# Optimization experiments

Measured on AMD Instinct MI355X. Metric: run time of the kernel, lower is better.

The kernel has to match this reference:

```python
import jax, jax.numpy as jnp
import numpy as np

B, N, E, C_IN, C_OUT = 4, 50000, 800000, 128, 128


def setup_inputs() -> dict:
    key = jax.random.key(0)
    k1, k2, k3, k4, k5 = jax.random.split(key, 5)
    x = jax.random.normal(k1, (B, N, C_IN), dtype=jnp.float32)
    edge_row = jax.random.randint(k2, (E,), 0, N, dtype=jnp.int32)
    edge_col = jax.random.randint(k3, (E,), 0, N, dtype=jnp.int32)
    edge_vals = jax.random.uniform(k4, (E,), dtype=jnp.float32)
    W = jax.random.normal(k5, (C_IN, C_OUT), dtype=jnp.float32) * 0.1  # weight_stddev=0.1
    b = jnp.full((C_OUT,), 0.1, dtype=jnp.float32)  # bias_constant=0.1
    return {"x": x, "edge_row": edge_row, "edge_col": edge_col,
            "edge_vals": edge_vals, "W": W, "b": b}


def reference(x, edge_row, edge_col, edge_vals, W, b):
    # Sparse adjacency aggregation: agg[b, r, :] = sum_e vals[e] * x[b, col[e], :]
    n = x.shape[1]

    def spmm(xb):  # xb: [N, C_in]
        msgs = xb[edge_col] * edge_vals[:, None]          # [E, C_in]
        return jax.ops.segment_sum(msgs, edge_row, num_segments=n)  # [N, C_in]

    agg = jax.vmap(spmm)(x)                               # [B, N, C_in]
    out = jnp.einsum('bnc,co->bno', agg, W) + b           # dense GEMM + bias
    return jax.nn.relu(out)
```

## Files before the change

### kernel.cpp

```cpp
#include <hip/hip_runtime.h>

#define NROWS 50000
#define BATCH 4
#define CH    128
#define CAP   64

typedef float  f32x4  __attribute__((ext_vector_type(4)));
typedef __bf16 bf16x8 __attribute__((ext_vector_type(8)));
typedef short  s16x8  __attribute__((ext_vector_type(8)));

static __device__ __forceinline__ unsigned short f2bf(float f) {
    unsigned u = __builtin_bit_cast(unsigned, f);
    u += 0x7fffu + ((u >> 16) & 1u);
    return (unsigned short)(u >> 16);
}

__global__ void k_scatter(const int* __restrict__ row, const int* __restrict__ col,
                          const float* __restrict__ vals, int E,
                          int* __restrict__ cnt, unsigned long long* __restrict__ csr) {
    int e = blockIdx.x * blockDim.x + threadIdx.x;
    if (e < E) {
        int r = row[e];
        int p = atomicAdd(&cnt[r], 1);
        if (p < CAP) {
            unsigned long long pk =
                (unsigned long long)(unsigned)col[e] |
                ((unsigned long long)__builtin_bit_cast(unsigned, vals[e]) << 32);
            csr[r * CAP + p] = pk;
        }
    }
}

__global__ __launch_bounds__(256) void k_xw(const float* __restrict__ x,
                                            const float* __restrict__ W,
                                            unsigned short* __restrict__ y) {
    __shared__ unsigned short WtL[128 * 136];
    __shared__ unsigned short yt[4][16 * 136];
    const int tid = threadIdx.x;
    for (int idx = tid; idx < 128 * 128; idx += 256) {
        int k = idx >> 7, n = idx & 127;
        WtL[n * 136 + k] = f2bf(W[idx]);
    }
    __syncthreads();

    const int wave = tid >> 6;
    const int lane = tid & 63;
    const int m    = lane & 15;
    const int quad = lane >> 4;
    unsigned short* __restrict__ myt = yt[wave];

    const int NSTRIP = (BATCH * NROWS) / 64;
    for (int s = blockIdx.x; s < NSTRIP; s += gridDim.x) {
        const int row0 = s * 64 + wave * 16;

        s16x8 a_s[4];
        const float* xr = x + (size_t)(row0 + m) * CH;
        #pragma unroll
        for (int kk = 0; kk < 4; ++kk) {
            const float4* p = (const float4*)(xr + kk * 32 + quad * 8);
            float4 f0 = p[0], f1 = p[1];
            s16x8 sv;
            sv[0] = f2bf(f0.x); sv[1] = f2bf(f0.y); sv[2] = f2bf(f0.z); sv[3] = f2bf(f0.w);
            sv[4] = f2bf(f1.x); sv[5] = f2bf(f1.y); sv[6] = f2bf(f1.z); sv[7] = f2bf(f1.w);
            a_s[kk] = sv;
        }

        #pragma unroll
        for (int nt = 0; nt < 8; ++nt) {
            f32x4 acc = {0.f, 0.f, 0.f, 0.f};
            #pragma unroll
            for (int kk = 0; kk < 4; ++kk) {
                bf16x8 b = *(const bf16x8*)&WtL[(nt * 16 + m) * 136 + kk * 32 + quad * 8];
                acc = __builtin_amdgcn_mfma_f32_16x16x32_bf16(
                          __builtin_bit_cast(bf16x8, a_s[kk]), b, acc, 0, 0, 0);
            }
            #pragma unroll
            for (int reg = 0; reg < 4; ++reg)
                myt[(quad * 4 + reg) * 136 + nt * 16 + m] = f2bf(acc[reg]);
        }

        #pragma unroll
        for (int it = 0; it < 4; ++it) {
            const int lrow = it * 4 + (lane >> 4);
            const int seg  = lane & 15;
            uint4 v = *(const uint4*)&myt[lrow * 136 + seg * 8];
            const int i  = row0 + lrow;
            const int bb = i / NROWS;
            const int n  = i - bb * NROWS;
            *(uint4*)&y[((size_t)n * BATCH + bb) * CH + seg * 8] = v;
        }
    }
}

template<int B0>
__global__ __launch_bounds__(128) void k_spmm_h(const unsigned* __restrict__ y,
                                                const int* __restrict__ cnt,
                                                const unsigned long long* __restrict__ csr,
                                                const float* __restrict__ bias,
                                                float* __restrict__ out) {
    __shared__ unsigned long long lcsr[CAP];
    const int r    = blockIdx.x;
    const int tid  = threadIdx.x;
    const int b    = B0 + (tid >> 6);
    const int lane = tid & 63;
    const int deg  = min(cnt[r], CAP);
    if (tid < deg) lcsr[tid] = csr[r * CAP + tid];
    __syncthreads();

    const unsigned* __restrict__ Y = y + b * (CH / 2) + lane;
    float ax = 0.f, ay = 0.f;
    int e = 0;
    for (; e + 8 <= deg; e += 8) {
        unsigned long long pk[8];
        unsigned u[8];
        #pragma unroll
        for (int j = 0; j < 8; ++j) pk[j] = lcsr[e + j];
        #pragma unroll
        for (int j = 0; j < 8; ++j) u[j] = Y[(size_t)(unsigned)pk[j] * 256];
        #pragma unroll
        for (int j = 0; j < 8; ++j) {
            float v = __builtin_bit_cast(float, (unsigned)(pk[j] >> 32));
            ax += v * __builtin_bit_cast(float, u[j] << 16);
            ay += v * __builtin_bit_cast(float, u[j] & 0xffff0000u);
        }
    }
    for (; e < deg; ++e) {
        unsigned long long pk = lcsr[e];
        float v = __builtin_bit_cast(float, (unsigned)(pk >> 32));
        unsigned u = Y[(size_t)(unsigned)pk * 256];
        ax += v * __builtin_bit_cast(float, u << 16);
        ay += v * __builtin_bit_cast(float, u & 0xffff0000u);
    }

    float2 bv = ((const float2*)bias)[lane];
    float ox = fmaxf(ax + bv.x, 0.f);
    float oy = fmaxf(ay + bv.y, 0.f);
    unsigned long long packed =
        (unsigned long long)__builtin_bit_cast(unsigned, ox) |
        ((unsigned long long)__builtin_bit_cast(unsigned, oy) << 32);
    unsigned long long* dst =
        (unsigned long long*)(out + ((size_t)b * NROWS + r) * CH) + lane;
    __builtin_nontemporal_store(packed, dst);
}

extern "C" void kernel_launch(void* const* d_in, const int* in_sizes, int n_in,
                              void* d_out, int out_size, void* d_ws, size_t ws_size,
                              hipStream_t stream) {
    const float* x        = (const float*)d_in[0];
    const int*   edge_row = (const int*)d_in[1];
    const int*   edge_col = (const int*)d_in[2];
    const float* edge_val = (const float*)d_in[3];
    const float* W        = (const float*)d_in[4];
    const float* bias     = (const float*)d_in[5];
    float*       out      = (float*)d_out;

    const int E = in_sizes[1];

    int*                cnt = (int*)d_ws;
    unsigned long long* csr = (unsigned long long*)(cnt + 50048);
    unsigned short*     y   = (unsigned short*)(csr + (size_t)NROWS * CAP);

    hipMemsetAsync(cnt, 0, 50048 * sizeof(int), stream);
    k_scatter<<<(E + 255) / 256, 256, 0, stream>>>(edge_row, edge_col, edge_val, E,
                                                   cnt, csr);
    k_xw<<<1250, 256, 0, stream>>>(x, W, y);
    k_spmm_h<0><<<NROWS, 128, 0, stream>>>((const unsigned*)y, cnt, csr, bias, out);
    k_spmm_h<2><<<NROWS, 128, 0, stream>>>((const unsigned*)y, cnt, csr, bias, out);
}
```

Before: 362.8 us.

## Write permuted bf16 layout from MFMA registers and fuse batch SpMM kernels

The XW kernel drops its LDS transpose staging and writes MFMA accumulator results directly to global memory in a permuted bf16 pair layout. The SpMM is merged into one kernel in which each wave handles one row across all four batches, with each lane gathering a 16-byte uint4 per edge instead of 4 bytes. This replaces two launches that each read the CSR, and the wider gather should cut gather instruction count. In exchange, output stores become scattered 4-byte nontemporal writes instead of 8-byte coalesced ones, and the strided channel permutation adds more complex indexing.

```diff
diff --git a/kernel.cpp b/kernel.cpp
--- a/kernel.cpp
+++ b/kernel.cpp
@@ -13,6 +13,9 @@
     unsigned u = __builtin_bit_cast(unsigned, f);
     u += 0x7fffu + ((u >> 16) & 1u);
     return (unsigned short)(u >> 16);
+}
+static __device__ __forceinline__ unsigned packbf(float lo, float hi) {
+    return (unsigned)f2bf(lo) | ((unsigned)f2bf(hi) << 16);
 }
 
 __global__ void k_scatter(const int* __restrict__ row, const int* __restrict__ col,
@@ -31,11 +34,10 @@
     }
 }
 
-__global__ __launch_bounds__(256) void k_xw(const float* __restrict__ x,
-                                            const float* __restrict__ W,
-                                            unsigned short* __restrict__ y) {
+__global__ __launch_bounds__(256, 4) void k_xw(const float* __restrict__ x,
+                                               const float* __restrict__ W,
+                                               unsigned* __restrict__ y) {
     __shared__ unsigned short WtL[128 * 136];
-    __shared__ unsigned short yt[4][16 * 136];
     const int tid = threadIdx.x;
     for (int idx = tid; idx < 128 * 128; idx += 256) {
         int k = idx >> 7, n = idx & 127;
@@ -47,7 +49,6 @@
     const int lane = tid & 63;
     const int m    = lane & 15;
     const int quad = lane >> 4;
-    unsigned short* __restrict__ myt = yt[wave];
 
     const int NSTRIP = (BATCH * NROWS) / 64;
     for (int s = blockIdx.x; s < NSTRIP; s += gridDim.x) {
@@ -65,82 +66,104 @@
             a_s[kk] = sv;
         }
 
+        unsigned uc[4][4];
         #pragma unroll
-        for (int nt = 0; nt < 8; ++nt) {
-            f32x4 acc = {0.f, 0.f, 0.f, 0.f};
+        for (int np = 0; np < 4; ++np) {
+            f32x4 acc0 = {0.f, 0.f, 0.f, 0.f};
+            f32x4 acc1 = {0.f, 0.f, 0.f, 0.f};
             #pragma unroll
             for (int kk = 0; kk < 4; ++kk) {
-                bf16x8 b = *(const bf16x8*)&WtL[(nt * 16 + m) * 136 + kk * 32 + quad * 8];
-                acc = __builtin_amdgcn_mfma_f32_16x16x32_bf16(
-                          __builtin_bit_cast(bf16x8, a_s[kk]), b, acc, 0, 0, 0);
+                bf16x8 b0 = *(const bf16x8*)&WtL[((2 * np) * 16 + m) * 136 + kk * 32 + quad * 8];
+                acc0 = __builtin_amdgcn_mfma_f32_16x16x32_bf16(
+                           __builtin_bit_cast(bf16x8, a_s[kk]), b0, acc0, 0, 0, 0);
+            }
+            #pragma unroll
+            for (int kk = 0; kk < 4; ++kk) {
+                bf16x8 b1 = *(const bf16x8*)&WtL[((2 * np + 1) * 16 + m) * 136 + kk * 32 + quad * 8];
+                acc1 = __builtin_amdgcn_mfma_f32_16x16x32_bf16(
+                           __builtin_bit_cast(bf16x8, a_s[kk]), b1, acc1, 0, 0, 0);
             }
             #pragma unroll
             for (int reg = 0; reg < 4; ++reg)
-                myt[(quad * 4 + reg) * 136 + nt * 16 + m] = f2bf(acc[reg]);
+                uc[reg][np] = packbf(acc0[reg], acc1[reg]);
         }
 
         #pragma unroll
-        for (int it = 0; it < 4; ++it) {
-            const int lrow = it * 4 + (lane >> 4);
-            const int seg  = lane & 15;
-            uint4 v = *(const uint4*)&myt[lrow * 136 + seg * 8];
-            const int i  = row0 + lrow;
+        for (int reg = 0; reg < 4; ++reg) {
+            const int i  = row0 + quad * 4 + reg;
             const int bb = i / NROWS;
             const int n  = i - bb * NROWS;
-            *(uint4*)&y[((size_t)n * BATCH + bb) * CH + seg * 8] = v;
+            uint4 v;
+            v.x = uc[reg][0]; v.y = uc[reg][1]; v.z = uc[reg][2]; v.w = uc[reg][3];
+            *(uint4*)&y[((size_t)n * 4 + bb) * 64 + m * 4] = v;
         }
     }
 }
 
-template<int B0>
-__global__ __launch_bounds__(128) void k_spmm_h(const unsigned* __restrict__ y,
-                                                const int* __restrict__ cnt,
-                                                const unsigned long long* __restrict__ csr,
-                                                const float* __restrict__ bias,
-                                                float* __restrict__ out) {
-    __shared__ unsigned long long lcsr[CAP];
-    const int r    = blockIdx.x;
+__global__ __launch_bounds__(256) void k_spmm(const uint4* __restrict__ y4,
+                                              const int* __restrict__ cnt,
+                                              const unsigned long long* __restrict__ csr,
+                                              const float* __restrict__ bias,
+                                              float* __restrict__ out) {
+    __shared__ unsigned long long lcsr[4][CAP];
     const int tid  = threadIdx.x;
-    const int b    = B0 + (tid >> 6);
+    const int wave = tid >> 6;
     const int lane = tid & 63;
+    const int b    = lane >> 4;
+    const int m    = lane & 15;
+    const int r    = blockIdx.x * 4 + wave;
     const int deg  = min(cnt[r], CAP);
-    if (tid < deg) lcsr[tid] = csr[r * CAP + tid];
+    if (lane < deg) lcsr[wave][lane] = csr[(size_t)r * CAP + lane];
     __syncthreads();
 
-    const unsigned* __restrict__ Y = y + b * (CH / 2) + lane;
-    float ax = 0.f, ay = 0.f;
+    const uint4* __restrict__ Yl = y4 + lane;
+    float ax[4] = {0.f, 0.f, 0.f, 0.f};
+    float ay[4] = {0.f, 0.f, 0.f, 0.f};
+
     int e = 0;
     for (; e + 8 <= deg; e += 8) {
         unsigned long long pk[8];
-        unsigned u[8];
         #pragma unroll
-        for (int j = 0; j < 8; ++j) pk[j] = lcsr[e + j];
+        for (int j = 0; j < 8; ++j) pk[j] = lcsr[wave][e + j];
+        uint4 u[8];
         #pragma unroll
-        for (int j = 0; j < 8; ++j) u[j] = Y[(size_t)(unsigned)pk[j] * 256];
+        for (int j = 0; j < 8; ++j) u[j] = Yl[(size_t)(unsigned)pk[j] * 64];
         #pragma unroll
         for (int j = 0; j < 8; ++j) {
             float v = __builtin_bit_cast(float, (unsigned)(pk[j] >> 32));
-            ax += v * __builtin_bit_cast(float, u[j] << 16);
-            ay += v * __builtin_bit_cast(float, u[j] & 0xffff0000u);
+            ax[0] += v * __builtin_bit_cast(float, u[j].x << 16);
+            ay[0] += v * __builtin_bit_cast(float, u[j].x & 0xffff0000u);
+            ax[1] += v * __builtin_bit_cast(float, u[j].y << 16);
+            ay[1] += v * __builtin_bit_cast(float, u[j].y & 0xffff0000u);
+            ax[2] += v * __builtin_bit_cast(float, u[j].z << 16);
+            ay[2] += v * __builtin_bit_cast(float, u[j].z & 0xffff0000u);
+            ax[3] += v * __builtin_bit_cast(float, u[j].w << 16);
+            ay[3] += v * __builtin_bit_cast(float, u[j].w & 0xffff0000u);
         }
     }
     for (; e < deg; ++e) {
-        unsigned long long pk = lcsr[e];
+        unsigned long long pk = lcsr[wave][e];
         float v = __builtin_bit_cast(float, (unsigned)(pk >> 32));
-        unsigned u = Y[(size_t)(unsigned)pk * 256];
-        ax += v * __builtin_bit_cast(float, u << 16);
-        ay += v * __builtin_bit_cast(float, u & 0xffff0000u);
+        uint4 u = Yl[(size_t)(unsigned)pk * 64];
+        ax[0] += v * __builtin_bit_cast(float, u.x << 16);
+        ay[0] += v * __builtin_bit_cast(float, u.x & 0xffff0000u);
+        ax[1] += v * __builtin_bit_cast(float, u.y << 16);
+        ay[1] += v * __builtin_bit_cast(float, u.y & 0xffff0000u);
+        ax[2] += v * __builtin_bit_cast(float, u.z << 16);
+        ay[2] += v * __builtin_bit_cast(float, u.z & 0xffff0000u);
+        ax[3] += v * __builtin_bit_cast(float, u.w << 16);
+        ay[3] += v * __builtin_bit_cast(float, u.w & 0xffff0000u);
     }
 
-    float2 bv = ((const float2*)bias)[lane];
-    float ox = fmaxf(ax + bv.x, 0.f);
-    float oy = fmaxf(ay + bv.y, 0.f);
-    unsigned long long packed =
-        (unsigned long long)__builtin_bit_cast(unsigned, ox) |
-        ((unsigned long long)__builtin_bit_cast(unsigned, oy) << 32);
-    unsigned long long* dst =
-        (unsigned long long*)(out + ((size_t)b * NROWS + r) * CH) + lane;
-    __builtin_nontemporal_store(packed, dst);
+    float* __restrict__ orow = out + ((size_t)b * NROWS + r) * CH;
+    #pragma unroll
+    for (int j = 0; j < 4; ++j) {
+        const int c0 = m + 32 * j;
+        float ox = fmaxf(ax[j] + bias[c0], 0.f);
+        float oy = fmaxf(ay[j] + bias[c0 + 16], 0.f);
+        __builtin_nontemporal_store(ox, orow + c0);
+        __builtin_nontemporal_store(oy, orow + c0 + 16);
+    }
 }
 
 extern "C" void kernel_launch(void* const* d_in, const int* in_sizes, int n_in,
@@ -158,12 +181,11 @@
 
     int*                cnt = (int*)d_ws;
     unsigned long long* csr = (unsigned long long*)(cnt + 50048);
-    unsigned short*     y   = (unsigned short*)(csr + (size_t)NROWS * CAP);
+    unsigned*           y   = (unsigned*)(csr + (size_t)NROWS * CAP);
 
     hipMemsetAsync(cnt, 0, 50048 * sizeof(int), stream);
     k_scatter<<<(E + 255) / 256, 256, 0, stream>>>(edge_row, edge_col, edge_val, E,
                                                    cnt, csr);
     k_xw<<<1250, 256, 0, stream>>>(x, W, y);
-    k_spmm_h<0><<<NROWS, 128, 0, stream>>>((const unsigned*)y, cnt, csr, bias, out);
-    k_spmm_h<2><<<NROWS, 128, 0, stream>>>((const unsigned*)y, cnt, csr, bias, out);
+    k_spmm<<<NROWS / 4, 256, 0, stream>>>((const uint4*)y, cnt, csr, bias, out);
 }
```

Result: slower. 402.1 us (+10.8%).

## Merge batch-split SpMM kernels into one wave-per-row kernel with 16-byte gathers

Applied to the files above, without the earlier changes.

Replaces the two half-batch SpMM launches, which used one block per row and 4-byte gathers, with a single launch where each wave owns one row. Each wave covers all four batches using 16-byte uint4 gathers from the bf16 Y buffer, so one 1 KB row of Y is read in a single load per lane. The CSR list is loaded once instead of twice, and launch count drops. Results are staged through shared memory so the output stores stay coalesced. The trade-off is more registers per lane and the extra shared-memory staging step.

```diff
diff --git a/kernel.cpp b/kernel.cpp
--- a/kernel.cpp
+++ b/kernel.cpp
@@ -92,55 +92,78 @@
     }
 }
 
-template<int B0>
-__global__ __launch_bounds__(128) void k_spmm_h(const unsigned* __restrict__ y,
-                                                const int* __restrict__ cnt,
-                                                const unsigned long long* __restrict__ csr,
-                                                const float* __restrict__ bias,
-                                                float* __restrict__ out) {
-    __shared__ unsigned long long lcsr[CAP];
-    const int r    = blockIdx.x;
+__global__ __launch_bounds__(256) void k_spmm(const uint4* __restrict__ y4,
+                                              const int* __restrict__ cnt,
+                                              const unsigned long long* __restrict__ csr,
+                                              const float* __restrict__ bias,
+                                              float* __restrict__ out) {
+    __shared__ unsigned long long lcsr[4][CAP];
+    __shared__ float lout[4][512];
     const int tid  = threadIdx.x;
-    const int b    = B0 + (tid >> 6);
+    const int wave = tid >> 6;
     const int lane = tid & 63;
+    const int b    = lane >> 4;
+    const int m    = lane & 15;
+    const int r    = blockIdx.x * 4 + wave;
     const int deg  = min(cnt[r], CAP);
-    if (tid < deg) lcsr[tid] = csr[r * CAP + tid];
+    if (lane < deg) lcsr[wave][lane] = csr[(size_t)r * CAP + lane];
     __syncthreads();
 
-    const unsigned* __restrict__ Y = y + b * (CH / 2) + lane;
-    float ax = 0.f, ay = 0.f;
+    const uint4* __restrict__ Yl = y4 + lane;
+    float alo[4] = {0.f, 0.f, 0.f, 0.f};
+    float ahi[4] = {0.f, 0.f, 0.f, 0.f};
+
     int e = 0;
     for (; e + 8 <= deg; e += 8) {
         unsigned long long pk[8];
-        unsigned u[8];
         #pragma unroll
-        for (int j = 0; j < 8; ++j) pk[j] = lcsr[e + j];
+        for (int j = 0; j < 8; ++j) pk[j] = lcsr[wave][e + j];
+        uint4 u[8];
         #pragma unroll
-        for (int j = 0; j < 8; ++j) u[j] = Y[(size_t)(unsigned)pk[j] * 256];
+        for (int j = 0; j < 8; ++j) u[j] = Yl[(size_t)(unsigned)pk[j] * 64];
         #pragma unroll
         for (int j = 0; j < 8; ++j) {
             float v = __builtin_bit_cast(float, (unsigned)(pk[j] >> 32));
-            ax += v * __builtin_bit_cast(float, u[j] << 16);
-            ay += v * __builtin_bit_cast(float, u[j] & 0xffff0000u);
+            alo[0] += v * __builtin_bit_cast(float, u[j].x << 16);
+            ahi[0] += v * __builtin_bit_cast(float, u[j].x & 0xffff0000u);
+            alo[1] += v * __builtin_bit_cast(float, u[j].y << 16);
+            ahi[1] += v * __builtin_bit_cast(float, u[j].y & 0xffff0000u);
+            alo[2] += v * __builtin_bit_cast(float, u[j].z << 16);
+            ahi[2] += v * __builtin_bit_cast(float, u[j].z & 0xffff0000u);
+            alo[3] += v * __builtin_bit_cast(float, u[j].w << 16);
+            ahi[3] += v * __builtin_bit_cast(float, u[j].w & 0xffff0000u);
         }
     }
     for (; e < deg; ++e) {
-        unsigned long long pk = lcsr[e];
+        unsigned long long pk = lcsr[wave][e];
         float v = __builtin_bit_cast(float, (unsigned)(pk >> 32));
-        unsigned u = Y[(size_t)(unsigned)pk * 256];
-        ax += v * __builtin_bit_cast(float, u << 16);
-        ay += v * __builtin_bit_cast(float, u & 0xffff0000u);
+        uint4 u = Yl[(size_t)(unsigned)pk * 64];
+        alo[0] += v * __builtin_bit_cast(float, u.x << 16);
+        ahi[0] += v * __builtin_bit_cast(float, u.x & 0xffff0000u);
+        alo[1] += v * __builtin_bit_cast(float, u.y << 16);
+        ahi[1] += v * __builtin_bit_cast(float, u.y & 0xffff0000u);
+        alo[2] += v * __builtin_bit_cast(float, u.z << 16);
+        ahi[2] += v * __builtin_bit_cast(float, u.z & 0xffff0000u);
+        alo[3] += v * __builtin_bit_cast(float, u.w << 16);
+        ahi[3] += v * __builtin_bit_cast(float, u.w & 0xffff0000u);
     }
 
-    float2 bv = ((const float2*)bias)[lane];
-    float ox = fmaxf(ax + bv.x, 0.f);
-    float oy = fmaxf(ay + bv.y, 0.f);
-    unsigned long long packed =
-        (unsigned long long)__builtin_bit_cast(unsigned, ox) |
-        ((unsigned long long)__builtin_bit_cast(unsigned, oy) << 32);
-    unsigned long long* dst =
-        (unsigned long long*)(out + ((size_t)b * NROWS + r) * CH) + lane;
-    __builtin_nontemporal_store(packed, dst);
+    #pragma unroll
+    for (int k = 0; k < 4; ++k) {
+        float2 bv = ((const float2*)bias)[4 * m + k];
+        float ox = fmaxf(alo[k] + bv.x, 0.f);
+        float oy = fmaxf(ahi[k] + bv.y, 0.f);
+        *(float2*)&lout[wave][b * 128 + 8 * m + 2 * k] = make_float2(ox, oy);
+    }
+
+    const int bb  = lane >> 4;
+    const int ch0 = (lane & 15) * 8;
+    float* __restrict__ orow = out + ((size_t)bb * NROWS + r) * CH + ch0;
+    #pragma unroll
+    for (int k = 0; k < 4; ++k) {
+        unsigned long long pv = *(const unsigned long long*)&lout[wave][lane * 8 + 2 * k];
+        __builtin_nontemporal_store(pv, (unsigned long long*)(orow + 2 * k));
+    }
 }
 
 extern "C" void kernel_launch(void* const* d_in, const int* in_sizes, int n_in,
@@ -164,6 +187,5 @@
     k_scatter<<<(E + 255) / 256, 256, 0, stream>>>(edge_row, edge_col, edge_val, E,
                                                    cnt, csr);
     k_xw<<<1250, 256, 0, stream>>>(x, W, y);
-    k_spmm_h<0><<<NROWS, 128, 0, stream>>>((const unsigned*)y, cnt, csr, bias, out);
-    k_spmm_h<2><<<NROWS, 128, 0, stream>>>((const unsigned*)y, cnt, csr, bias, out);
+    k_spmm<<<NROWS / 4, 256, 0, stream>>>((const uint4*)y, cnt, csr, bias, out);
 }
```

Measured after the change: 367.7 us. About the same (+1.3%).
